# Kernel optimization log

Measured on AMD Instinct MI355X. Metric: run time of the kernel, lower is better.

Reference implementation:

```python
import jax, jax.numpy as jnp
import numpy as np

VAR_XY = 0.1  # SSD encoding variances
VAR_WH = 0.2


def _iou(truths, priors):
    # truths [G,4], priors [P,4] in corner form (x1,y1,x2,y2) -> [G,P]
    lt = jnp.maximum(truths[:, None, :2], priors[None, :, :2])
    rb = jnp.minimum(truths[:, None, 2:], priors[None, :, 2:])
    wh = jnp.clip(rb - lt, 0.0, None)
    inter = wh[..., 0] * wh[..., 1]
    area_t = (truths[:, 2] - truths[:, 0]) * (truths[:, 3] - truths[:, 1])
    area_p = (priors[:, 2] - priors[:, 0]) * (priors[:, 3] - priors[:, 1])
    return inter / (area_t[:, None] + area_p[None, :] - inter)


def _encode(truths, matched):
    # truths [G,1,4], matched priors [G,k,4], corner form -> SSD offsets [G,k,4]
    p_cxcy = (matched[..., :2] + matched[..., 2:]) * 0.5
    p_wh = matched[..., 2:] - matched[..., :2]
    g_cxcy = (truths[..., :2] + truths[..., 2:]) * 0.5
    g_wh = truths[..., 2:] - truths[..., :2]
    off_xy = (g_cxcy - p_cxcy) / (VAR_XY * p_wh)
    off_wh = jnp.log(g_wh / p_wh) / VAR_WH
    return jnp.concatenate([off_xy, off_wh], axis=-1)


def setup_inputs() -> dict:
    key = jax.random.key(0)
    k1, k2, k3, k4 = jax.random.split(key, 4)
    B, P, G = 16, 32768, 128
    # priors: valid corner-form boxes built from centers + sizes
    p_c = jax.random.uniform(k1, (B, P, 2), minval=0.1, maxval=0.9)
    p_s = jax.random.uniform(k2, (B, P, 2), minval=0.02, maxval=0.3)
    priors = jnp.concatenate([p_c - p_s * 0.5, p_c + p_s * 0.5], axis=-1)
    rpn_rois = jnp.stack([priors, priors], axis=1)  # [B,2,P,4]; channel 1 used
    # GT boxes, valid corner form
    t_c = jax.random.uniform(k3, (B, G, 2), minval=0.1, maxval=0.9)
    t_s = jax.random.uniform(k4, (B, G, 2), minval=0.05, maxval=0.4)
    targets = jnp.concatenate([t_c - t_s * 0.5, t_c + t_s * 0.5], axis=-1)
    return {"rpn_rois": rpn_rois, "targets": targets, "expand_num": 4}


def reference(rpn_rois, targets, expand_num):
    defaults = rpn_rois[:, 1]  # [B,P,4]

    def per_image(truths, priors):
        ious = _iou(truths, priors)                      # [G,P]
        _, idx = jax.lax.top_k(ious, expand_num)         # [G,k] best priors per GT
        matched = priors[idx]                            # [G,k,4]
        off = _encode(truths[:, None, :], matched)       # [G,k,4]
        return off.reshape(-1, 4)                        # [G*k,4]

    return jax.vmap(per_image)(targets, defaults)        # [B, G*k, 4]
```

## Files before the change

kernel.cpp:

```cpp
#include <hip/hip_runtime.h>

#define B 16
#define P 32768
#define NG 128
#define KTOP 4
#define NBX 32
#define NBY 32
#define NBB (NBX * NBY)
#define SUB 16
#define SUBP (P / SUB)
typedef unsigned long long u64;
typedef unsigned int u32;

__device__ __forceinline__ int bkt(float v) {
    int k = (int)((v + 0.08f) * 32.0f);
    return k < 0 ? 0 : (k > 31 ? 31 : k);
}

__device__ __forceinline__ void ceu(u64 &x, u64 &y) {
    u64 a = x, b = y; bool gt = a > b;
    x = gt ? a : b;  y = gt ? b : a;
}
__device__ __forceinline__ void cef(float &x, float &y) {
    float h = fmaxf(x, y), l = fminf(x, y); x = h; y = l;
}

#define INS4(x, a0, a1, a2, a3)                                   \
    {                                                             \
        bool g0 = (x) > a0, g1 = (x) > a1, g2 = (x) > a2, g3 = (x) > a3; \
        u64 n3 = g2 ? a2 : (g3 ? (x) : a3);                       \
        u64 n2 = g1 ? a1 : (g2 ? (x) : a2);                       \
        u64 n1 = g0 ? a0 : (g1 ? (x) : a1);                       \
        u64 n0 = g0 ? (x) : a0;                                   \
        a0 = n0; a1 = n1; a2 = n2; a3 = n3;                       \
    }

#define IOUKEY(q, oi, dst)                                        \
    {                                                             \
        float ap = ((q).z - (q).x) * ((q).w - (q).y);             \
        float ltx = fmaxf(t0, (q).x), lty = fmaxf(t1, (q).y);     \
        float rbx = fminf(t2, (q).z), rby = fminf(t3, (q).w);     \
        float wx = fmaxf(rbx - ltx, 0.0f);                        \
        float wy = fmaxf(rby - lty, 0.0f);                        \
        float inter = wx * wy;                                    \
        float iou = inter / ((areaT + ap) - inter);               \
        dst = ((u64)__float_as_uint(iou) << 32) | (u32)(~(oi));   \
    }

__global__ __launch_bounds__(256)
void k_hist(const float* __restrict__ rois, u32* __restrict__ cnt, float* __restrict__ whm)
{
    const int b = blockIdx.x >> 4, sub = blockIdx.x & 15;
    const int tid = threadIdx.x;
    __shared__ u32 h[NBB];
    __shared__ float red[8];
    for (int j = tid; j < NBB; j += 256) h[j] = 0;
    __syncthreads();

    const float4* __restrict__ pv = (const float4*)(rois + ((size_t)(2 * b + 1)) * P * 4);
    float wmax = 0.f, hmax = 0.f;
    #pragma unroll
    for (int it = 0; it < SUBP / 256; ++it) {
        float4 q = pv[sub * SUBP + it * 256 + tid];
        atomicAdd(&h[bkt(q.x) * NBY + bkt(q.y)], 1u);
        wmax = fmaxf(wmax, q.z - q.x);
        hmax = fmaxf(hmax, q.w - q.y);
    }
    #pragma unroll
    for (int d = 32; d >= 1; d >>= 1) {
        wmax = fmaxf(wmax, __shfl_down(wmax, d, 64));
        hmax = fmaxf(hmax, __shfl_down(hmax, d, 64));
    }
    if ((tid & 63) == 0) { red[(tid >> 6) * 2] = wmax; red[(tid >> 6) * 2 + 1] = hmax; }
    __syncthreads();
    for (int j = tid; j < NBB; j += 256) cnt[(size_t)blockIdx.x * NBB + j] = h[j];
    if (tid == 0) {
        whm[blockIdx.x * 2 + 0] = fmaxf(fmaxf(red[0], red[2]), fmaxf(red[4], red[6]));
        whm[blockIdx.x * 2 + 1] = fmaxf(fmaxf(red[1], red[3]), fmaxf(red[5], red[7]));
    }
}

__global__ __launch_bounds__(256)
void k_scat(const float* __restrict__ rois, const u32* __restrict__ cnt,
            float4* __restrict__ sbox, u32* __restrict__ sidx, u32* __restrict__ off)
{
    const int b = blockIdx.x >> 4, sub = blockIdx.x & 15;
    const int tid = threadIdx.x;
    const int lane = tid & 63, wv = tid >> 6;
    __shared__ u32 cur[NBB];
    __shared__ u32 wpart[4];

    u32 bintot[4] = {0, 0, 0, 0};
    u32 below[4]  = {0, 0, 0, 0};
    #pragma unroll
    for (int k = 0; k < SUB; ++k) {
        #pragma unroll
        for (int m = 0; m < 4; ++m) {
            u32 v = cnt[(size_t)(b * SUB + k) * NBB + 4 * tid + m];
            bintot[m] += v;
            if (k < sub) below[m] += v;
        }
    }
    u32 s_local = bintot[0] + bintot[1] + bintot[2] + bintot[3];
    u32 incl = s_local;
    #pragma unroll
    for (int d = 1; d < 64; d <<= 1) {
        u32 v = __shfl_up(incl, d, 64);
        if (lane >= d) incl += v;
    }
    if (lane == 63) wpart[wv] = incl;
    __syncthreads();
    u32 wbase = 0;
    #pragma unroll
    for (int w = 0; w < 4; ++w) if (w < wv) wbase += wpart[w];

    u32 run = wbase + incl - s_local;
    #pragma unroll
    for (int m = 0; m < 4; ++m) {
        cur[4 * tid + m] = run + below[m];
        if (sub == 0) off[b * (NBB + 1) + 4 * tid + m] = run;
        run += bintot[m];
    }
    if (sub == 0 && tid == 0) off[b * (NBB + 1) + NBB] = P;
    __syncthreads();

    const float4* __restrict__ pv = (const float4*)(rois + ((size_t)(2 * b + 1)) * P * 4);
    #pragma unroll
    for (int it = 0; it < SUBP / 256; ++it) {
        int i = sub * SUBP + it * 256 + tid;
        float4 q = pv[i];
        u32 slot = atomicAdd(&cur[bkt(q.x) * NBY + bkt(q.y)], 1u);
        sbox[(size_t)b * P + slot] = q;
        sidx[(size_t)b * P + slot] = (u32)i;
    }
}

__global__ __launch_bounds__(256, 4)
void k_main(const float* __restrict__ rois, const float* __restrict__ targets,
            const float4* __restrict__ sbox, const u32* __restrict__ sidx,
            const u32* __restrict__ off, const float* __restrict__ whm,
            float* __restrict__ out)
{
    #pragma clang fp contract(off)

    const int blk = blockIdx.x;
    const int b   = ((blk & 7) << 1) | ((blk >> 3) & 1);
    const int g   = blk >> 4;
    const int tid = threadIdx.x;
    const int lane = tid & 63, wv = tid >> 6;

    const float* tp = targets + ((size_t)(b * NG + g)) * 4;
    const float t0 = tp[0], t1 = tp[1], t2 = tp[2], t3 = tp[3];
    const float areaT = (t2 - t0) * (t3 - t1);
    const float gw = t2 - t0, gh = t3 - t1;

    const float4* __restrict__ boxb = sbox + (size_t)b * P;
    const u32*    __restrict__ idxb = sidx + (size_t)b * P;
    const u32*    __restrict__ offb = off + b * (NBB + 1);

    __shared__ float sf[4][4];
    __shared__ u64   sm[4][4];
    __shared__ int   seg_lo[NBX], seg_hi[NBX];

    float w0 = -1.f, w1 = -1.f, w2 = -1.f, w3 = -1.f;
    #pragma unroll
    for (int it = 0; it < 8; ++it) {
        float4 q = boxb[(it * 4 + wv) * (P / 32) + lane];
        float ap = (q.z - q.x) * (q.w - q.y);
        float ltx = fmaxf(t0, q.x), lty = fmaxf(t1, q.y);
        float rbx = fminf(t2, q.z), rby = fminf(t3, q.w);
        float wx = fmaxf(rbx - ltx, 0.0f);
        float wy = fmaxf(rby - lty, 0.0f);
        float inter = wx * wy;
        float iou = inter / ((areaT + ap) - inter);
        float x = iou, hh;
        hh = fmaxf(w0, x); x = fminf(w0, x); w0 = hh;
        hh = fmaxf(w1, x); x = fminf(w1, x); w1 = hh;
        hh = fmaxf(w2, x); x = fminf(w2, x); w2 = hh;
        w3 = fmaxf(w3, x);
    }
    #pragma unroll
    for (int d = 32; d >= 1; d >>= 1) {
        float n0 = __shfl_down(w0, d, 64);
        float n1 = __shfl_down(w1, d, 64);
        float n2 = __shfl_down(w2, d, 64);
        float n3 = __shfl_down(w3, d, 64);
        cef(w0, n3); cef(w1, n2); cef(w2, n1); cef(w3, n0);
        cef(w0, w2); cef(w1, w3); cef(w0, w1); cef(w2, w3);
    }
    if (lane == 0) { sf[wv][0] = w0; sf[wv][1] = w1; sf[wv][2] = w2; sf[wv][3] = w3; }
    __syncthreads();

    if (wv == 0) {
        float m0 = -1.f, m1 = -1.f, m2 = -1.f, m3 = -1.f;
        #pragma unroll
        for (int j = 0; j < 16; ++j) {
            float x = sf[j >> 2][j & 3], hh;
            hh = fmaxf(m0, x); x = fminf(m0, x); m0 = hh;
            hh = fmaxf(m1, x); x = fminf(m1, x); m1 = hh;
            hh = fmaxf(m2, x); x = fminf(m2, x); m2 = hh;
            m3 = fmaxf(m3, x);
        }
        float wm = 0.f, hm = 0.f;
        #pragma unroll
        for (int k = 0; k < SUB; ++k) {
            wm = fmaxf(wm, whm[(b * SUB + k) * 2 + 0]);
            hm = fmaxf(hm, whm[(b * SUB + k) * 2 + 1]);
        }
        float lb = m3 * 0.999f;
        int bxlo = 0, bxhi = 31, bylo = 0, byhi = 31;
        if (lb > 1e-6f) {
            bxlo = bkt(t0 + lb * gw - wm - 1e-5f);
            bxhi = bkt(t2 - lb * gw + 1e-5f);
            bylo = bkt(t1 + lb * gh - hm - 1e-5f);
            byhi = bkt(t3 - lb * gh + 1e-5f);
        }
        if (lane < NBX) {
            bool inx = (lane >= bxlo) && (lane <= bxhi);
            int lo = (int)offb[lane * NBY + bylo];
            int hi = (int)offb[lane * NBY + byhi + 1];
            seg_lo[lane] = lo;
            seg_hi[lane] = inx ? hi : lo;
        }
    }
    __syncthreads();

    u64 a0 = 0, a1 = 0, a2 = 0, a3 = 0;
    u64 c0 = 0, c1 = 0, c2 = 0, c3 = 0;
    for (int s = wv; s < NBX; s += 4) {
        const int lo = seg_lo[s];
        const int n = seg_hi[s] - lo;
        const float4* __restrict__ bp = boxb + lo;
        const u32*    __restrict__ ip = idxb + lo;

        float4 qa0 = {0,0,0,0}, qb0 = {0,0,0,0}, qa1 = {0,0,0,0}, qb1 = {0,0,0,0};
        u32 oa0 = 0, ob0 = 0, oa1 = 0, ob1 = 0;
        if (lane < n)       { qa0 = bp[lane];       oa0 = ip[lane]; }
        if (lane + 64 < n)  { qb0 = bp[lane + 64];  ob0 = ip[lane + 64]; }
        if (lane + 128 < n) { qa1 = bp[lane + 128]; oa1 = ip[lane + 128]; }
        if (lane + 192 < n) { qb1 = bp[lane + 192]; ob1 = ip[lane + 192]; }

        for (int base = 0; base < n; base += 128) {
            float4 qa2 = qa1, qb2 = qb1; u32 oa2 = oa1, ob2 = ob1;
            const int ja = base + 256 + lane, jb = base + 320 + lane;
            if (ja < n) { qa2 = bp[ja]; oa2 = ip[ja]; }
            if (jb < n) { qb2 = bp[jb]; ob2 = ip[jb]; }

            if (base + lane < n) {
                u64 x; IOUKEY(qa0, oa0, x);
                INS4(x, a0, a1, a2, a3);
            }
            if (base + 64 + lane < n) {
                u64 x; IOUKEY(qb0, ob0, x);
                INS4(x, c0, c1, c2, c3);
            }
            qa0 = qa1; oa0 = oa1; qb0 = qb1; ob0 = ob1;
            qa1 = qa2; oa1 = oa2; qb1 = qb2; ob1 = ob2;
        }
    }
    ceu(a0, c3); ceu(a1, c2); ceu(a2, c1); ceu(a3, c0);
    ceu(a0, a2); ceu(a1, a3); ceu(a0, a1); ceu(a2, a3);

    #pragma unroll
    for (int d = 32; d >= 1; d >>= 1) {
        u64 n0 = __shfl_down(a0, d, 64);
        u64 n1 = __shfl_down(a1, d, 64);
        u64 n2 = __shfl_down(a2, d, 64);
        u64 n3 = __shfl_down(a3, d, 64);
        ceu(a0, n3); ceu(a1, n2); ceu(a2, n1); ceu(a3, n0);
        ceu(a0, a2); ceu(a1, a3); ceu(a0, a1); ceu(a2, a3);
    }
    if (lane == 0) { sm[wv][0] = a0; sm[wv][1] = a1; sm[wv][2] = a2; sm[wv][3] = a3; }
    __syncthreads();

    if (tid == 0) {
        u64 f0 = 0, f1 = 0, f2 = 0, f3 = 0;
        #pragma unroll
        for (int j = 0; j < 16; ++j) {
            u64 x = sm[j >> 2][j & 3];
            INS4(x, f0, f1, f2, f3);
        }
        const float gcx = (t0 + t2) * 0.5f;
        const float gcy = (t1 + t3) * 0.5f;
        const float4* __restrict__ pv =
            (const float4*)(rois + ((size_t)(2 * b + 1)) * P * 4);
        float4* __restrict__ o4 = (float4*)out;

        u64 ks[KTOP] = {f0, f1, f2, f3};
        #pragma unroll
        for (int k = 0; k < KTOP; ++k) {
            int idx = (int)(~(u32)ks[k]) & (P - 1);
            float4 q = pv[idx];
            float pcx = (q.x + q.z) * 0.5f;
            float pcy = (q.y + q.w) * 0.5f;
            float pw  = q.z - q.x;
            float ph  = q.w - q.y;
            float4 r;
            r.x = (gcx - pcx) / (0.1f * pw);
            r.y = (gcy - pcy) / (0.1f * ph);
            r.z = logf(gw / pw) / 0.2f;
            r.w = logf(gh / ph) / 0.2f;
            o4[((size_t)(b * NG + g)) * KTOP + k] = r;
        }
    }
}

extern "C" void kernel_launch(void* const* d_in, const int* in_sizes, int n_in,
                              void* d_out, int out_size, void* d_ws, size_t ws_size,
                              hipStream_t stream) {
    const float* rois    = (const float*)d_in[0];
    const float* targets = (const float*)d_in[1];
    float* out = (float*)d_out;

    char* w = (char*)d_ws;
    float4* sbox = (float4*)(w);
    u32*    sidx = (u32*)  (w + (size_t)B * P * 16);
    u32*    cnt  = (u32*)  (w + (size_t)B * P * 20);
    u32*    off  = (u32*)  (w + (size_t)B * P * 24);
    float*  whm  = (float*)(w + (size_t)B * P * 24 + 66560);

    k_hist<<<dim3(B * SUB), dim3(256), 0, stream>>>(rois, cnt, whm);
    k_scat<<<dim3(B * SUB), dim3(256), 0, stream>>>(rois, cnt, sbox, sidx, off);
    k_main<<<dim3(B * NG),  dim3(256), 0, stream>>>(rois, targets, sbox, sidx, off, whm, out);
}
```

Measured before the change: 122.5 us.

## Replace spatial-bucket pruning with tiled brute-force scan using sampled IoU threshold

Removes the histogram and scatter bucketing kernels. Each image's priors are now cut into shared-memory tiles, and each block computes IoU for all 128 GTs against a tile. A first kernel samples 2048 priors to estimate a per-GT 4th-best IoU threshold, which gates the expensive divide and insert. Per-tile top-4 partials are then merged in a final reduction kernel. This trades spatial pruning for dense, regular compute with reuse of priors across all GTs, and it does about 4M IoU evaluations per image instead of a pruned subset.

New measurement: 118.5 us. 1.03x faster.

```diff
diff --git a/kernel.cpp b/kernel.cpp
--- a/kernel.cpp
+++ b/kernel.cpp
@@ -4,18 +4,12 @@
 #define P 32768
 #define NG 128
 #define KTOP 4
-#define NBX 32
-#define NBY 32
-#define NBB (NBX * NBY)
-#define SUB 16
-#define SUBP (P / SUB)
+#define TILE 512
+#define NT (P / TILE)
+#define SAMP 2048
+
 typedef unsigned long long u64;
 typedef unsigned int u32;
-
-__device__ __forceinline__ int bkt(float v) {
-    int k = (int)((v + 0.08f) * 32.0f);
-    return k < 0 ? 0 : (k > 31 ? 31 : k);
-}
 
 __device__ __forceinline__ void ceu(u64 &x, u64 &y) {
     u64 a = x, b = y; bool gt = a > b;
@@ -35,140 +29,27 @@
         a0 = n0; a1 = n1; a2 = n2; a3 = n3;                       \
     }
 
-#define IOUKEY(q, oi, dst)                                        \
-    {                                                             \
-        float ap = ((q).z - (q).x) * ((q).w - (q).y);             \
-        float ltx = fmaxf(t0, (q).x), lty = fmaxf(t1, (q).y);     \
-        float rbx = fminf(t2, (q).z), rby = fminf(t3, (q).w);     \
-        float wx = fmaxf(rbx - ltx, 0.0f);                        \
-        float wy = fmaxf(rby - lty, 0.0f);                        \
-        float inter = wx * wy;                                    \
-        float iou = inter / ((areaT + ap) - inter);               \
-        dst = ((u64)__float_as_uint(iou) << 32) | (u32)(~(oi));   \
-    }
-
 __global__ __launch_bounds__(256)
-void k_hist(const float* __restrict__ rois, u32* __restrict__ cnt, float* __restrict__ whm)
-{
-    const int b = blockIdx.x >> 4, sub = blockIdx.x & 15;
-    const int tid = threadIdx.x;
-    __shared__ u32 h[NBB];
-    __shared__ float red[8];
-    for (int j = tid; j < NBB; j += 256) h[j] = 0;
-    __syncthreads();
-
-    const float4* __restrict__ pv = (const float4*)(rois + ((size_t)(2 * b + 1)) * P * 4);
-    float wmax = 0.f, hmax = 0.f;
-    #pragma unroll
-    for (int it = 0; it < SUBP / 256; ++it) {
-        float4 q = pv[sub * SUBP + it * 256 + tid];
-        atomicAdd(&h[bkt(q.x) * NBY + bkt(q.y)], 1u);
-        wmax = fmaxf(wmax, q.z - q.x);
-        hmax = fmaxf(hmax, q.w - q.y);
-    }
-    #pragma unroll
-    for (int d = 32; d >= 1; d >>= 1) {
-        wmax = fmaxf(wmax, __shfl_down(wmax, d, 64));
-        hmax = fmaxf(hmax, __shfl_down(hmax, d, 64));
-    }
-    if ((tid & 63) == 0) { red[(tid >> 6) * 2] = wmax; red[(tid >> 6) * 2 + 1] = hmax; }
-    __syncthreads();
-    for (int j = tid; j < NBB; j += 256) cnt[(size_t)blockIdx.x * NBB + j] = h[j];
-    if (tid == 0) {
-        whm[blockIdx.x * 2 + 0] = fmaxf(fmaxf(red[0], red[2]), fmaxf(red[4], red[6]));
-        whm[blockIdx.x * 2 + 1] = fmaxf(fmaxf(red[1], red[3]), fmaxf(red[5], red[7]));
-    }
-}
-
-__global__ __launch_bounds__(256)
-void k_scat(const float* __restrict__ rois, const u32* __restrict__ cnt,
-            float4* __restrict__ sbox, u32* __restrict__ sidx, u32* __restrict__ off)
-{
-    const int b = blockIdx.x >> 4, sub = blockIdx.x & 15;
-    const int tid = threadIdx.x;
-    const int lane = tid & 63, wv = tid >> 6;
-    __shared__ u32 cur[NBB];
-    __shared__ u32 wpart[4];
-
-    u32 bintot[4] = {0, 0, 0, 0};
-    u32 below[4]  = {0, 0, 0, 0};
-    #pragma unroll
-    for (int k = 0; k < SUB; ++k) {
-        #pragma unroll
-        for (int m = 0; m < 4; ++m) {
-            u32 v = cnt[(size_t)(b * SUB + k) * NBB + 4 * tid + m];
-            bintot[m] += v;
-            if (k < sub) below[m] += v;
-        }
-    }
-    u32 s_local = bintot[0] + bintot[1] + bintot[2] + bintot[3];
-    u32 incl = s_local;
-    #pragma unroll
-    for (int d = 1; d < 64; d <<= 1) {
-        u32 v = __shfl_up(incl, d, 64);
-        if (lane >= d) incl += v;
-    }
-    if (lane == 63) wpart[wv] = incl;
-    __syncthreads();
-    u32 wbase = 0;
-    #pragma unroll
-    for (int w = 0; w < 4; ++w) if (w < wv) wbase += wpart[w];
-
-    u32 run = wbase + incl - s_local;
-    #pragma unroll
-    for (int m = 0; m < 4; ++m) {
-        cur[4 * tid + m] = run + below[m];
-        if (sub == 0) off[b * (NBB + 1) + 4 * tid + m] = run;
-        run += bintot[m];
-    }
-    if (sub == 0 && tid == 0) off[b * (NBB + 1) + NBB] = P;
-    __syncthreads();
-
-    const float4* __restrict__ pv = (const float4*)(rois + ((size_t)(2 * b + 1)) * P * 4);
-    #pragma unroll
-    for (int it = 0; it < SUBP / 256; ++it) {
-        int i = sub * SUBP + it * 256 + tid;
-        float4 q = pv[i];
-        u32 slot = atomicAdd(&cur[bkt(q.x) * NBY + bkt(q.y)], 1u);
-        sbox[(size_t)b * P + slot] = q;
-        sidx[(size_t)b * P + slot] = (u32)i;
-    }
-}
-
-__global__ __launch_bounds__(256, 4)
-void k_main(const float* __restrict__ rois, const float* __restrict__ targets,
-            const float4* __restrict__ sbox, const u32* __restrict__ sidx,
-            const u32* __restrict__ off, const float* __restrict__ whm,
-            float* __restrict__ out)
+void k_tau(const float* __restrict__ rois, const float* __restrict__ targets,
+           float* __restrict__ tau)
 {
     #pragma clang fp contract(off)
-
     const int blk = blockIdx.x;
-    const int b   = ((blk & 7) << 1) | ((blk >> 3) & 1);
-    const int g   = blk >> 4;
-    const int tid = threadIdx.x;
-    const int lane = tid & 63, wv = tid >> 6;
-
-    const float* tp = targets + ((size_t)(b * NG + g)) * 4;
-    const float t0 = tp[0], t1 = tp[1], t2 = tp[2], t3 = tp[3];
-    const float areaT = (t2 - t0) * (t3 - t1);
-    const float gw = t2 - t0, gh = t3 - t1;
-
-    const float4* __restrict__ boxb = sbox + (size_t)b * P;
-    const u32*    __restrict__ idxb = sidx + (size_t)b * P;
-    const u32*    __restrict__ offb = off + b * (NBB + 1);
+    const int b = blk >> 7, g = blk & (NG - 1);
+    const int tid = threadIdx.x, lane = tid & 63, wv = tid >> 6;
+
+    const float4 t = *(const float4*)(targets + ((size_t)(b * NG + g)) * 4);
+    const float areaT = (t.z - t.x) * (t.w - t.y);
+    const float4* __restrict__ pv = (const float4*)(rois + ((size_t)(2 * b + 1)) * P * 4);
 
     __shared__ float sf[4][4];
-    __shared__ u64   sm[4][4];
-    __shared__ int   seg_lo[NBX], seg_hi[NBX];
-
     float w0 = -1.f, w1 = -1.f, w2 = -1.f, w3 = -1.f;
     #pragma unroll
-    for (int it = 0; it < 8; ++it) {
-        float4 q = boxb[(it * 4 + wv) * (P / 32) + lane];
+    for (int it = 0; it < SAMP / 256; ++it) {
+        float4 q = pv[it * 256 + tid];
         float ap = (q.z - q.x) * (q.w - q.y);
-        float ltx = fmaxf(t0, q.x), lty = fmaxf(t1, q.y);
-        float rbx = fminf(t2, q.z), rby = fminf(t3, q.w);
+        float ltx = fmaxf(t.x, q.x), lty = fmaxf(t.y, q.y);
+        float rbx = fminf(t.z, q.z), rby = fminf(t.w, q.w);
         float wx = fmaxf(rbx - ltx, 0.0f);
         float wy = fmaxf(rby - lty, 0.0f);
         float inter = wx * wy;
@@ -190,8 +71,7 @@
     }
     if (lane == 0) { sf[wv][0] = w0; sf[wv][1] = w1; sf[wv][2] = w2; sf[wv][3] = w3; }
     __syncthreads();
-
-    if (wv == 0) {
+    if (tid == 0) {
         float m0 = -1.f, m1 = -1.f, m2 = -1.f, m3 = -1.f;
         #pragma unroll
         for (int j = 0; j < 16; ++j) {
@@ -201,66 +81,81 @@
             hh = fmaxf(m2, x); x = fminf(m2, x); m2 = hh;
             m3 = fmaxf(m3, x);
         }
-        float wm = 0.f, hm = 0.f;
-        #pragma unroll
-        for (int k = 0; k < SUB; ++k) {
-            wm = fmaxf(wm, whm[(b * SUB + k) * 2 + 0]);
-            hm = fmaxf(hm, whm[(b * SUB + k) * 2 + 1]);
+        tau[blk] = m3;
+    }
+}
+
+__global__ __launch_bounds__(256, 4)
+void k_scan(const float* __restrict__ rois, const float* __restrict__ targets,
+            const float* __restrict__ tau, u64* __restrict__ part)
+{
+    #pragma clang fp contract(off)
+    const int blk = blockIdx.x;
+    const int b = blk / NT, tile = blk & (NT - 1);
+    const int tid = threadIdx.x;
+    const int g = tid & (NG - 1), hf = tid >> 7;
+
+    __shared__ float4 sQ[TILE];
+    __shared__ float  sA[TILE];
+    __shared__ u64    sm[NG][4];
+
+    const float4* __restrict__ pv =
+        (const float4*)(rois + ((size_t)(2 * b + 1)) * P * 4) + (size_t)tile * TILE;
+    for (int i = tid; i < TILE; i += 256) {
+        float4 q = pv[i];
+        sQ[i] = q;
+        sA[i] = (q.z - q.x) * (q.w - q.y);
+    }
+
+    const float4 t = *(const float4*)(targets + ((size_t)(b * NG + g)) * 4);
+    const float areaT = (t.z - t.x) * (t.w - t.y);
+    const float tv   = tau[b * NG + g];
+    const float taum = tv * (1.0f - 1e-4f);
+    const float fc   = (1.0f + tv) * (1.0f + 1e-4f);
+    const float cA   = taum * areaT;
+    __syncthreads();
+
+    u64 a0 = 0, a1 = 0, a2 = 0, a3 = 0;
+    const int base = hf * (TILE / 2);
+    const u32 gidx = (u32)(tile * TILE + base);
+    #pragma unroll 4
+    for (int j = 0; j < TILE / 2; ++j) {
+        const float4 q = sQ[base + j];
+        const float ap = sA[base + j];
+        float ltx = fmaxf(t.x, q.x), lty = fmaxf(t.y, q.y);
+        float rbx = fminf(t.z, q.z), rby = fminf(t.w, q.w);
+        float wx = fmaxf(rbx - ltx, 0.0f);
+        float wy = fmaxf(rby - lty, 0.0f);
+        float inter = wx * wy;
+        if (inter * fc >= __builtin_fmaf(taum, ap, cA)) {
+            float iou = inter / ((areaT + ap) - inter);
+            u64 x = ((u64)__float_as_uint(iou) << 32) | (u32)(~(gidx + (u32)j));
+            INS4(x, a0, a1, a2, a3);
         }
-        float lb = m3 * 0.999f;
-        int bxlo = 0, bxhi = 31, bylo = 0, byhi = 31;
-        if (lb > 1e-6f) {
-            bxlo = bkt(t0 + lb * gw - wm - 1e-5f);
-            bxhi = bkt(t2 - lb * gw + 1e-5f);
-            bylo = bkt(t1 + lb * gh - hm - 1e-5f);
-            byhi = bkt(t3 - lb * gh + 1e-5f);
-        }
-        if (lane < NBX) {
-            bool inx = (lane >= bxlo) && (lane <= bxhi);
-            int lo = (int)offb[lane * NBY + bylo];
-            int hi = (int)offb[lane * NBY + byhi + 1];
-            seg_lo[lane] = lo;
-            seg_hi[lane] = inx ? hi : lo;
-        }
-    }
+    }
+
+    if (hf == 1) { sm[g][0] = a0; sm[g][1] = a1; sm[g][2] = a2; sm[g][3] = a3; }
     __syncthreads();
-
-    u64 a0 = 0, a1 = 0, a2 = 0, a3 = 0;
-    u64 c0 = 0, c1 = 0, c2 = 0, c3 = 0;
-    for (int s = wv; s < NBX; s += 4) {
-        const int lo = seg_lo[s];
-        const int n = seg_hi[s] - lo;
-        const float4* __restrict__ bp = boxb + lo;
-        const u32*    __restrict__ ip = idxb + lo;
-
-        float4 qa0 = {0,0,0,0}, qb0 = {0,0,0,0}, qa1 = {0,0,0,0}, qb1 = {0,0,0,0};
-        u32 oa0 = 0, ob0 = 0, oa1 = 0, ob1 = 0;
-        if (lane < n)       { qa0 = bp[lane];       oa0 = ip[lane]; }
-        if (lane + 64 < n)  { qb0 = bp[lane + 64];  ob0 = ip[lane + 64]; }
-        if (lane + 128 < n) { qa1 = bp[lane + 128]; oa1 = ip[lane + 128]; }
-        if (lane + 192 < n) { qb1 = bp[lane + 192]; ob1 = ip[lane + 192]; }
-
-        for (int base = 0; base < n; base += 128) {
-            float4 qa2 = qa1, qb2 = qb1; u32 oa2 = oa1, ob2 = ob1;
-            const int ja = base + 256 + lane, jb = base + 320 + lane;
-            if (ja < n) { qa2 = bp[ja]; oa2 = ip[ja]; }
-            if (jb < n) { qb2 = bp[jb]; ob2 = ip[jb]; }
-
-            if (base + lane < n) {
-                u64 x; IOUKEY(qa0, oa0, x);
-                INS4(x, a0, a1, a2, a3);
-            }
-            if (base + 64 + lane < n) {
-                u64 x; IOUKEY(qb0, ob0, x);
-                INS4(x, c0, c1, c2, c3);
-            }
-            qa0 = qa1; oa0 = oa1; qb0 = qb1; ob0 = ob1;
-            qa1 = qa2; oa1 = oa2; qb1 = qb2; ob1 = ob2;
-        }
-    }
-    ceu(a0, c3); ceu(a1, c2); ceu(a2, c1); ceu(a3, c0);
-    ceu(a0, a2); ceu(a1, a3); ceu(a0, a1); ceu(a2, a3);
-
+    if (hf == 0) {
+        u64 b0 = sm[g][0], b1 = sm[g][1], b2 = sm[g][2], b3 = sm[g][3];
+        ceu(a0, b3); ceu(a1, b2); ceu(a2, b1); ceu(a3, b0);
+        ceu(a0, a2); ceu(a1, a3); ceu(a0, a1); ceu(a2, a3);
+        u64* dst = part + (((size_t)b * NT + tile) * NG + g) * KTOP;
+        dst[0] = a0; dst[1] = a1; dst[2] = a2; dst[3] = a3;
+    }
+}
+
+__global__ __launch_bounds__(64)
+void k_top(const float* __restrict__ rois, const float* __restrict__ targets,
+           const u64* __restrict__ part, float* __restrict__ out)
+{
+    #pragma clang fp contract(off)
+    const int blk = blockIdx.x;
+    const int b = blk >> 7, g = blk & (NG - 1);
+    const int lane = threadIdx.x;
+
+    const u64* __restrict__ src = part + (((size_t)b * NT + lane) * NG + g) * KTOP;
+    u64 a0 = src[0], a1 = src[1], a2 = src[2], a3 = src[3];
     #pragma unroll
     for (int d = 32; d >= 1; d >>= 1) {
         u64 n0 = __shfl_down(a0, d, 64);
@@ -270,23 +165,17 @@
         ceu(a0, n3); ceu(a1, n2); ceu(a2, n1); ceu(a3, n0);
         ceu(a0, a2); ceu(a1, a3); ceu(a0, a1); ceu(a2, a3);
     }
-    if (lane == 0) { sm[wv][0] = a0; sm[wv][1] = a1; sm[wv][2] = a2; sm[wv][3] = a3; }
-    __syncthreads();
-
-    if (tid == 0) {
-        u64 f0 = 0, f1 = 0, f2 = 0, f3 = 0;
-        #pragma unroll
-        for (int j = 0; j < 16; ++j) {
-            u64 x = sm[j >> 2][j & 3];
-            INS4(x, f0, f1, f2, f3);
-        }
+    if (lane == 0) {
+        const float4 t = *(const float4*)(targets + ((size_t)(b * NG + g)) * 4);
+        const float t0 = t.x, t1 = t.y, t2 = t.z, t3 = t.w;
+        const float gw = t2 - t0, gh = t3 - t1;
         const float gcx = (t0 + t2) * 0.5f;
         const float gcy = (t1 + t3) * 0.5f;
         const float4* __restrict__ pv =
             (const float4*)(rois + ((size_t)(2 * b + 1)) * P * 4);
         float4* __restrict__ o4 = (float4*)out;
 
-        u64 ks[KTOP] = {f0, f1, f2, f3};
+        u64 ks[KTOP] = {a0, a1, a2, a3};
         #pragma unroll
         for (int k = 0; k < KTOP; ++k) {
             int idx = (int)(~(u32)ks[k]) & (P - 1);
@@ -312,14 +201,10 @@
     const float* targets = (const float*)d_in[1];
     float* out = (float*)d_out;
 
-    char* w = (char*)d_ws;
-    float4* sbox = (float4*)(w);
-    u32*    sidx = (u32*)  (w + (size_t)B * P * 16);
-    u32*    cnt  = (u32*)  (w + (size_t)B * P * 20);
-    u32*    off  = (u32*)  (w + (size_t)B * P * 24);
-    float*  whm  = (float*)(w + (size_t)B * P * 24 + 66560);
-
-    k_hist<<<dim3(B * SUB), dim3(256), 0, stream>>>(rois, cnt, whm);
-    k_scat<<<dim3(B * SUB), dim3(256), 0, stream>>>(rois, cnt, sbox, sidx, off);
-    k_main<<<dim3(B * NG),  dim3(256), 0, stream>>>(rois, targets, sbox, sidx, off, whm, out);
-}
+    float* tau  = (float*)d_ws;
+    u64*   part = (u64*)((char*)d_ws + 8192);
+
+    k_tau <<<dim3(B * NG), dim3(256), 0, stream>>>(rois, targets, tau);
+    k_scan<<<dim3(B * NT), dim3(256), 0, stream>>>(rois, targets, tau, part);
+    k_top <<<dim3(B * NG), dim3(64),  0, stream>>>(rois, targets, part, out);
+}
```
